# Kernel tuning notes

Hardware: AMD Instinct MI355X
Metric: run time of the kernel (lower is better)

Reference implementation:

```python
import jax, jax.numpy as jnp
import numpy as np
from jax import lax

EPS = 1e-5


def _conv3x3(x, w):
    # NCHW input, OIHW weight, stride 1, padding 1
    return lax.conv_general_dilated(
        x, w, window_strides=(1, 1), padding=((1, 1), (1, 1)),
        dimension_numbers=("NCHW", "OIHW", "NCHW"))


def _batchnorm(y, gamma, beta):
    # training-mode BN: batch statistics over N,H,W
    mean = jnp.mean(y, axis=(0, 2, 3), keepdims=True)
    var = jnp.var(y, axis=(0, 2, 3), keepdims=True)
    inv = lax.rsqrt(var + EPS)
    return (y - mean) * inv * gamma[None, :, None, None] + beta[None, :, None, None]


def setup_inputs() -> dict:
    key = jax.random.key(0)
    k1, k2, k3 = jax.random.split(key, 3)
    N, C, H, W = 32, 128, 56, 56
    x = jax.random.normal(k1, (N, C, H, W), dtype=jnp.float32)
    w1 = jax.random.normal(k2, (C, C, 3, 3), dtype=jnp.float32) * 0.05
    w2 = jax.random.normal(k3, (C, C, 3, 3), dtype=jnp.float32) * 0.05
    gamma1 = jnp.ones((C,), jnp.float32)
    beta1 = jnp.zeros((C,), jnp.float32)
    gamma2 = jnp.ones((C,), jnp.float32)
    beta2 = jnp.zeros((C,), jnp.float32)
    return {"x": x, "w1": w1, "gamma1": gamma1, "beta1": beta1,
            "w2": w2, "gamma2": gamma2, "beta2": beta2}


def reference(x, w1, gamma1, beta1, w2, gamma2, beta2):
    # binarized conv weights: sign(w), with straight-through estimator
    # (matches torch's .data swap, which routes grads to the original weight)
    w1b = w1 + lax.stop_gradient(jnp.sign(w1) - w1)
    w2b = w2 + lax.stop_gradient(jnp.sign(w2) - w2)
    out = jax.nn.relu(_batchnorm(_conv3x3(x, w1b), gamma1, beta1))
    out = _batchnorm(_conv3x3(out, w2b), gamma2, beta2)
    out = out + x  # identity shortcut (stride=1, in_planes==planes)
    return jax.nn.relu(out)
```

## Files before the change

### kernel.cpp

```cpp
#include <hip/hip_runtime.h>

typedef unsigned short u16;
typedef unsigned short u16x8 __attribute__((ext_vector_type(8)));
typedef __bf16 bf16x8 __attribute__((ext_vector_type(8)));
typedef float f32x4 __attribute__((ext_vector_type(4)));

#define HW 3136
#define NPIX 100352
#define PADR 3364
#define KD 1152

__device__ __forceinline__ float bf2f(u16 u) {
    unsigned int x = ((unsigned int)u) << 16;
    return __builtin_bit_cast(float, x);
}
__device__ __forceinline__ u16 f2bf(float f) {
    unsigned int u = __builtin_bit_cast(unsigned int, f);
    return (u16)((u + 0x7FFFu + ((u >> 16) & 1u)) >> 16);
}
__device__ __forceinline__ void gload16(const void* g, void* l) {
    __builtin_amdgcn_global_load_lds(
        (const __attribute__((address_space(1))) unsigned int*)g,
        (__attribute__((address_space(3))) unsigned int*)l, 16, 0, 0);
}

__global__ void setup_kernel(const float* __restrict__ w1, const float* __restrict__ w2,
                             u16* __restrict__ Bm1, u16* __restrict__ Bm2,
                             u16* __restrict__ xbp) {
    const int b = blockIdx.x;
    const int t = threadIdx.x;
    if (b < 1152) {
        const float* w = (b < 576) ? w1 : w2;
        u16* Bm = (b < 576) ? Bm1 : Bm2;
        int i = (b % 576) * 256 + t;
        int k  = i / KD;
        int kk = i - k * KD;
        int c  = kk & 127;
        int rs = kk >> 7;
        float v = w[(size_t)(k * 128 + c) * 9 + rs];
        float sv = (v > 0.f) ? 1.f : ((v < 0.f) ? -1.f : 0.f);
        Bm[i] = f2bf(sv);
    } else {
        int idx = (b - 1152) * 256 + t;
        int pix = idx >> 4;
        int cc  = idx & 15;
        int n  = pix / 228;
        int pb = pix - n * 228;
        int h, w;
        if (pb < 58)       { h = 0;  w = pb; }
        else if (pb < 116) { h = 57; w = pb - 58; }
        else { int q = pb - 116; h = 1 + (q >> 1); w = (q & 1) ? 57 : 0; }
        u16x8 z = {};
        *(u16x8*)(xbp + ((size_t)(n * PADR + h * 58 + w)) * 128 + cc * 8) = z;
    }
}

__global__ void x_to_nhwc(const float* __restrict__ x, u16* __restrict__ xbp) {
    __shared__ float tile[32][65];
    const int t = threadIdx.x;
    const int n = blockIdx.y;
    const int ct = blockIdx.x & 3;
    const int pt = blockIdx.x >> 2;
    const int c0 = ct * 32, p0 = pt * 64;
    {
        const int c  = t >> 3;
        const int pw = (t & 7) * 8;
        const size_t ib = ((size_t)(n * 128 + c0 + c)) * HW + p0 + pw;
        const float4 v0 = *(const float4*)(x + ib);
        const float4 v1 = *(const float4*)(x + ib + 4);
        tile[c][pw + 0] = v0.x; tile[c][pw + 1] = v0.y;
        tile[c][pw + 2] = v0.z; tile[c][pw + 3] = v0.w;
        tile[c][pw + 4] = v1.x; tile[c][pw + 5] = v1.y;
        tile[c][pw + 6] = v1.z; tile[c][pw + 7] = v1.w;
    }
    __syncthreads();
    {
        const int pl = t >> 2;
        const int cs = (t & 3) * 8;
        const int p  = p0 + pl;
        const int h  = p / 56;
        const int w  = p - h * 56;
        u16x8 o;
#pragma unroll
        for (int j = 0; j < 8; ++j) o[j] = f2bf(tile[cs + j][pl]);
        *(u16x8*)(xbp + ((size_t)(n * PADR + (h + 1) * 58 + (w + 1))) * 128 + c0 + cs) = o;
    }
}

#define A0 0
#define B0 8192
#define A1 16384
#define B1 24576

__global__ __launch_bounds__(256, 2) void conv_mfma(
    const u16* __restrict__ xbp, const u16* __restrict__ Bm,
    u16* __restrict__ y, float2* __restrict__ partial)
{
    __shared__ __align__(16) u16 smem[32768];
    const int t = threadIdx.x;
    const int bid = blockIdx.x;
    const int pm0 = bid * 128;
    const int wid  = t >> 6;
    const int lane = t & 63;
    const int lrow = lane & 15;
    const int lhk  = lane >> 4;
    const int m0 = (wid >> 1) * 64;
    const int n0 = (wid & 1) * 64;

    const int rsub = lane >> 3;
    const int csrc = (lane & 7) ^ rsub;
    int apix[4], bbase[4];
#pragma unroll
    for (int j = 0; j < 4; ++j) {
        int row = (wid * 4 + j) * 8 + rsub;
        int ps  = pm0 + row;
        int n   = ps / HW;
        int rem = ps - n * HW;
        int h   = rem / 56;
        int w   = rem - h * 56;
        apix[j]  = (n * PADR + (h + 1) * 58 + (w + 1)) * 128 + csrc * 8;
        bbase[j] = row * KD + csrc * 8;
    }

    f32x4 acc[4][4] = {};

#define STAGE(AOFF, BOFF, p) do {                                              \
    int rs_ = (p) >> 1; int r_ = rs_ / 3; int s_ = rs_ - r_ * 3;               \
    int ash = ((r_ - 1) * 58 + (s_ - 1)) * 128 + ((p) & 1) * 64;               \
    int bsh = (p) * 64;                                                        \
    _Pragma("unroll")                                                          \
    for (int j = 0; j < 4; ++j) {                                              \
        gload16(xbp + apix[j] + ash, smem + (AOFF) + (wid * 4 + j) * 512);     \
        gload16(Bm + bbase[j] + bsh, smem + (BOFF) + (wid * 4 + j) * 512);     \
    } } while (0)

#define COMPUTE(AOFF, BOFF) do {                                               \
    _Pragma("unroll")                                                          \
    for (int kc = 0; kc < 2; ++kc) {                                           \
        bf16x8 af[4], bv[4];                                                   \
        _Pragma("unroll")                                                      \
        for (int mi = 0; mi < 4; ++mi) {                                       \
            int ck = (((kc << 2) | lhk) ^ (lrow & 7)) << 3;                    \
            af[mi] = *(const bf16x8*)&smem[(AOFF) + (m0 + mi * 16 + lrow) * 64 + ck]; \
        }                                                                      \
        _Pragma("unroll")                                                      \
        for (int ni = 0; ni < 4; ++ni) {                                       \
            int ck = (((kc << 2) | lhk) ^ (lrow & 7)) << 3;                    \
            bv[ni] = *(const bf16x8*)&smem[(BOFF) + (n0 + ni * 16 + lrow) * 64 + ck]; \
        }                                                                      \
        __builtin_amdgcn_s_setprio(1);                                         \
        _Pragma("unroll")                                                      \
        for (int mi = 0; mi < 4; ++mi)                                         \
        _Pragma("unroll")                                                      \
            for (int ni = 0; ni < 4; ++ni)                                     \
                acc[mi][ni] = __builtin_amdgcn_mfma_f32_16x16x32_bf16(         \
                    af[mi], bv[ni], acc[mi][ni], 0, 0, 0);                     \
        __builtin_amdgcn_s_setprio(0);                                         \
    } } while (0)

    STAGE(A0, B0, 0);
    __syncthreads();
#pragma unroll 1
    for (int pp = 0; pp < 18; pp += 2) {
        STAGE(A1, B1, pp + 1);
        COMPUTE(A0, B0);
        __syncthreads();
        if (pp < 16) STAGE(A0, B0, pp + 2);
        COMPUTE(A1, B1);
        __syncthreads();
    }
#undef STAGE
#undef COMPUTE

    float sv[4], qv[4];
#pragma unroll
    for (int ni = 0; ni < 4; ++ni) {
        float a = 0.f, b = 0.f;
#pragma unroll
        for (int mi = 0; mi < 4; ++mi)
#pragma unroll
            for (int q = 0; q < 4; ++q) { float v = acc[mi][ni][q]; a += v; b += v * v; }
        a += __shfl_xor(a, 16); a += __shfl_xor(a, 32);
        b += __shfl_xor(b, 16); b += __shfl_xor(b, 32);
        sv[ni] = a; qv[ni] = b;
    }
    float2* sred = (float2*)(smem + 20480);
    if (lane < 16) {
#pragma unroll
        for (int ni = 0; ni < 4; ++ni)
            sred[wid * 64 + ni * 16 + lane] = make_float2(sv[ni], qv[ni]);
    }

#pragma unroll
    for (int mi = 0; mi < 4; ++mi)
#pragma unroll
        for (int ni = 0; ni < 4; ++ni)
#pragma unroll
            for (int q = 0; q < 4; ++q)
                smem[(m0 + mi * 16 + lhk * 4 + q) * 136 + n0 + ni * 16 + lrow] =
                    f2bf(acc[mi][ni][q]);
    __syncthreads();
    {
        const int px = t >> 1, half = t & 1;
        const u16* src = &smem[px * 136 + half * 64];
        u16* dst = y + (size_t)(pm0 + px) * 128 + half * 64;
#pragma unroll
        for (int j = 0; j < 8; ++j)
            *(u16x8*)(dst + j * 8) = *(const u16x8*)(src + j * 8);
    }
    if (t < 128) {
        const int ni = (t >> 4) & 3, oc = t & 15, hi = t >> 6;
        float2 u = sred[hi * 64 + ni * 16 + oc];
        float2 v = sred[(hi + 2) * 64 + ni * 16 + oc];
        partial[(size_t)t * 784 + bid] = make_float2(u.x + v.x, u.y + v.y);
    }
}

__global__ void stats_finalize(const float2* __restrict__ partial,
                               const float* __restrict__ gamma, const float* __restrict__ beta,
                               float2* __restrict__ coef) {
    __shared__ float ss[256], ss2[256];
    const int c = blockIdx.x, t = threadIdx.x;
    const float2* pc = partial + (size_t)c * 784;
    float s = 0.f, s2 = 0.f;
    for (int i = t; i < 784; i += 256) { float2 v = pc[i]; s += v.x; s2 += v.y; }
    ss[t] = s; ss2[t] = s2;
    __syncthreads();
    for (int o = 128; o > 0; o >>= 1) {
        if (t < o) { ss[t] += ss[t + o]; ss2[t] += ss2[t + o]; }
        __syncthreads();
    }
    if (t == 0) {
        double mean = (double)ss[0] / (double)NPIX;
        double var  = (double)ss2[0] / (double)NPIX - mean * mean;
        if (var < 0.0) var = 0.0;
        float inv = rsqrtf((float)var + 1e-5f);
        float a = gamma[c] * inv;
        coef[c] = make_float2(a, beta[c] - (float)mean * a);
    }
}

__global__ void bnrelu_kernel(const u16* __restrict__ y, const float2* __restrict__ coef,
                              u16* __restrict__ xbp) {
    __shared__ float2 sc[128];
    const int t = threadIdx.x;
    if (t < 128) sc[t] = coef[t];
    __syncthreads();
    size_t i = (size_t)blockIdx.x * 256 + t;
    u16x8 v = *(const u16x8*)(y + i * 8);
    int p  = (int)(i >> 4);
    int c0 = (int)(i & 15) * 8;
    int n   = p / HW;
    int rem = p - n * HW;
    int h   = rem / 56;
    int w   = rem - h * 56;
    u16x8 o;
#pragma unroll
    for (int j = 0; j < 8; ++j) {
        float2 k = sc[c0 + j];
        o[j] = f2bf(fmaxf(bf2f(v[j]) * k.x + k.y, 0.f));
    }
    *(u16x8*)(xbp + ((size_t)(n * PADR + (h + 1) * 58 + (w + 1))) * 128 + c0) = o;
}

__global__ void bn_add_relu_nchw(const u16* __restrict__ y2, const float2* __restrict__ coef,
                                 const float* __restrict__ x, float* __restrict__ out) {
    __shared__ float tile[32][65];
    __shared__ float2 sc[32];
    const int t = threadIdx.x;
    const int n = blockIdx.y;
    const int ct = blockIdx.x & 3;
    const int pt = blockIdx.x >> 2;
    const int c0 = ct * 32, p0 = pt * 64;
    if (t < 32) sc[t] = coef[c0 + t];
    __syncthreads();
    {
        const int p  = t >> 2;
        const int cs = (t & 3) * 8;
        const u16x8 v = *(const u16x8*)(y2 + ((size_t)(n * HW + p0 + p)) * 128 + c0 + cs);
#pragma unroll
        for (int j = 0; j < 8; ++j) {
            float2 k = sc[cs + j];
            tile[cs + j][p] = bf2f(v[j]) * k.x + k.y;
        }
    }
    __syncthreads();
    {
        const int c  = t >> 3;
        const int pw = (t & 7) * 8;
        const size_t ob = ((size_t)(n * 128 + c0 + c)) * HW + p0 + pw;
        const float4 x0 = *(const float4*)(x + ob);
        const float4 x1 = *(const float4*)(x + ob + 4);
        float4 o0, o1;
        o0.x = fmaxf(tile[c][pw + 0] + x0.x, 0.f);
        o0.y = fmaxf(tile[c][pw + 1] + x0.y, 0.f);
        o0.z = fmaxf(tile[c][pw + 2] + x0.z, 0.f);
        o0.w = fmaxf(tile[c][pw + 3] + x0.w, 0.f);
        o1.x = fmaxf(tile[c][pw + 4] + x1.x, 0.f);
        o1.y = fmaxf(tile[c][pw + 5] + x1.y, 0.f);
        o1.z = fmaxf(tile[c][pw + 6] + x1.z, 0.f);
        o1.w = fmaxf(tile[c][pw + 7] + x1.w, 0.f);
        *(float4*)(out + ob) = o0;
        *(float4*)(out + ob + 4) = o1;
    }
}

extern "C" void kernel_launch(void* const* d_in, const int* in_sizes, int n_in,
                              void* d_out, int out_size, void* d_ws, size_t ws_size,
                              hipStream_t stream) {
    const float* x  = (const float*)d_in[0];
    const float* w1 = (const float*)d_in[1];
    const float* g1 = (const float*)d_in[2];
    const float* b1 = (const float*)d_in[3];
    const float* w2 = (const float*)d_in[4];
    const float* g2 = (const float*)d_in[5];
    const float* b2 = (const float*)d_in[6];
    float* out = (float*)d_out;
    char* ws = (char*)d_ws;

    u16*    xbp  = (u16*)(ws);
    u16*    ybuf = (u16*)(ws + 27557888);
    u16*    Bm1  = (u16*)(ws + 53248000);
    u16*    Bm2  = (u16*)(ws + 53542912);
    float2* part = (float2*)(ws + 53837824);
    float2* cf1  = (float2*)(ws + 54640640);
    float2* cf2  = (float2*)(ws + 54641664);

    setup_kernel<<<1608, 256, 0, stream>>>(w1, w2, Bm1, Bm2, xbp);
    x_to_nhwc<<<dim3(196, 32), 256, 0, stream>>>(x, xbp);

    conv_mfma<<<784, 256, 0, stream>>>(xbp, Bm1, ybuf, part);
    stats_finalize<<<128, 256, 0, stream>>>(part, g1, b1, cf1);
    bnrelu_kernel<<<6272, 256, 0, stream>>>(ybuf, cf1, xbp);

    conv_mfma<<<784, 256, 0, stream>>>(xbp, Bm2, ybuf, part);
    stats_finalize<<<128, 256, 0, stream>>>(part, g2, b2, cf2);
    bn_add_relu_nchw<<<dim3(196, 32), 256, 0, stream>>>(ybuf, cf2, x, out);
}
```

Baseline: 148.5 us.

## Deepen conv LDS pipeline with vmcnt waits and read residual from bf16 NHWC

The conv main loop now keeps two stages of global_load_lds in flight. It uses explicit s_waitcnt vmcnt(8)/s_barrier pairs instead of __syncthreads, so loads for the next stage overlap the MFMA compute of the current one. The BN+ReLU intermediate is written into the output buffer as a padded scratch area, with extra blocks zeroing its border. This keeps the bf16 NHWC copy of x intact. The final kernel then reads the residual from that bf16 copy instead of the fp32 NCHW x, cutting memory traffic but adding bf16 rounding to the residual.

```diff
diff --git a/kernel.cpp b/kernel.cpp
--- a/kernel.cpp
+++ b/kernel.cpp
@@ -158,19 +158,34 @@
         __builtin_amdgcn_s_setprio(0);                                         \
     } } while (0)
 
+#define WAITBAR8() asm volatile("s_waitcnt vmcnt(8)\n\ts_barrier" ::: "memory")
+#define WAITBAR0() asm volatile("s_waitcnt vmcnt(0)\n\ts_barrier" ::: "memory")
+#define BAR()      asm volatile("s_barrier" ::: "memory")
+
     STAGE(A0, B0, 0);
-    __syncthreads();
+    STAGE(A1, B1, 1);
 #pragma unroll 1
-    for (int pp = 0; pp < 18; pp += 2) {
-        STAGE(A1, B1, pp + 1);
+    for (int pp = 0; pp < 16; pp += 2) {
+        WAITBAR8();
         COMPUTE(A0, B0);
-        __syncthreads();
-        if (pp < 16) STAGE(A0, B0, pp + 2);
+        BAR();
+        STAGE(A0, B0, pp + 2);
+        WAITBAR8();
         COMPUTE(A1, B1);
-        __syncthreads();
-    }
+        BAR();
+        STAGE(A1, B1, pp + 3);
+    }
+    WAITBAR8();
+    COMPUTE(A0, B0);
+    BAR();
+    WAITBAR0();
+    COMPUTE(A1, B1);
+    BAR();
 #undef STAGE
 #undef COMPUTE
+#undef WAITBAR8
+#undef WAITBAR0
+#undef BAR
 
     float sv[4], qv[4];
 #pragma unroll
@@ -241,12 +256,27 @@
 }
 
 __global__ void bnrelu_kernel(const u16* __restrict__ y, const float2* __restrict__ coef,
-                              u16* __restrict__ xbp) {
+                              u16* __restrict__ out1p) {
     __shared__ float2 sc[128];
-    const int t = threadIdx.x;
+    const int b = blockIdx.x;
+    const int t = threadIdx.x;
+    if (b >= 6272) {
+        int idx = (b - 6272) * 256 + t;
+        int pix = idx >> 4;
+        int cc  = idx & 15;
+        int n  = pix / 228;
+        int pb = pix - n * 228;
+        int h, w;
+        if (pb < 58)       { h = 0;  w = pb; }
+        else if (pb < 116) { h = 57; w = pb - 58; }
+        else { int q = pb - 116; h = 1 + (q >> 1); w = (q & 1) ? 57 : 0; }
+        u16x8 z = {};
+        *(u16x8*)(out1p + ((size_t)(n * PADR + h * 58 + w)) * 128 + cc * 8) = z;
+        return;
+    }
     if (t < 128) sc[t] = coef[t];
     __syncthreads();
-    size_t i = (size_t)blockIdx.x * 256 + t;
+    size_t i = (size_t)b * 256 + t;
     u16x8 v = *(const u16x8*)(y + i * 8);
     int p  = (int)(i >> 4);
     int c0 = (int)(i & 15) * 8;
@@ -260,11 +290,11 @@
         float2 k = sc[c0 + j];
         o[j] = f2bf(fmaxf(bf2f(v[j]) * k.x + k.y, 0.f));
     }
-    *(u16x8*)(xbp + ((size_t)(n * PADR + (h + 1) * 58 + (w + 1))) * 128 + c0) = o;
+    *(u16x8*)(out1p + ((size_t)(n * PADR + (h + 1) * 58 + (w + 1))) * 128 + c0) = o;
 }
 
 __global__ void bn_add_relu_nchw(const u16* __restrict__ y2, const float2* __restrict__ coef,
-                                 const float* __restrict__ x, float* __restrict__ out) {
+                                 const u16* __restrict__ xbp, float* __restrict__ out) {
     __shared__ float tile[32][65];
     __shared__ float2 sc[32];
     const int t = threadIdx.x;
@@ -275,13 +305,18 @@
     if (t < 32) sc[t] = coef[c0 + t];
     __syncthreads();
     {
-        const int p  = t >> 2;
+        const int pl = t >> 2;
         const int cs = (t & 3) * 8;
-        const u16x8 v = *(const u16x8*)(y2 + ((size_t)(n * HW + p0 + p)) * 128 + c0 + cs);
+        const int p  = p0 + pl;
+        const int h  = p / 56;
+        const int w  = p - h * 56;
+        const u16x8 v = *(const u16x8*)(y2 + ((size_t)(n * HW + p)) * 128 + c0 + cs);
+        const u16x8 xv = *(const u16x8*)(xbp +
+            ((size_t)(n * PADR + (h + 1) * 58 + (w + 1))) * 128 + c0 + cs);
 #pragma unroll
         for (int j = 0; j < 8; ++j) {
             float2 k = sc[cs + j];
-            tile[cs + j][p] = bf2f(v[j]) * k.x + k.y;
+            tile[cs + j][pl] = bf2f(v[j]) * k.x + k.y + bf2f(xv[j]);
         }
     }
     __syncthreads();
@@ -289,17 +324,15 @@
         const int c  = t >> 3;
         const int pw = (t & 7) * 8;
         const size_t ob = ((size_t)(n * 128 + c0 + c)) * HW + p0 + pw;
-        const float4 x0 = *(const float4*)(x + ob);
-        const float4 x1 = *(const float4*)(x + ob + 4);
         float4 o0, o1;
-        o0.x = fmaxf(tile[c][pw + 0] + x0.x, 0.f);
-        o0.y = fmaxf(tile[c][pw + 1] + x0.y, 0.f);
-        o0.z = fmaxf(tile[c][pw + 2] + x0.z, 0.f);
-        o0.w = fmaxf(tile[c][pw + 3] + x0.w, 0.f);
-        o1.x = fmaxf(tile[c][pw + 4] + x1.x, 0.f);
-        o1.y = fmaxf(tile[c][pw + 5] + x1.y, 0.f);
-        o1.z = fmaxf(tile[c][pw + 6] + x1.z, 0.f);
-        o1.w = fmaxf(tile[c][pw + 7] + x1.w, 0.f);
+        o0.x = fmaxf(tile[c][pw + 0], 0.f);
+        o0.y = fmaxf(tile[c][pw + 1], 0.f);
+        o0.z = fmaxf(tile[c][pw + 2], 0.f);
+        o0.w = fmaxf(tile[c][pw + 3], 0.f);
+        o1.x = fmaxf(tile[c][pw + 4], 0.f);
+        o1.y = fmaxf(tile[c][pw + 5], 0.f);
+        o1.z = fmaxf(tile[c][pw + 6], 0.f);
+        o1.w = fmaxf(tile[c][pw + 7], 0.f);
         *(float4*)(out + ob) = o0;
         *(float4*)(out + ob + 4) = o1;
     }
@@ -318,22 +351,23 @@
     float* out = (float*)d_out;
     char* ws = (char*)d_ws;
 
-    u16*    xbp  = (u16*)(ws);
-    u16*    ybuf = (u16*)(ws + 27557888);
-    u16*    Bm1  = (u16*)(ws + 53248000);
-    u16*    Bm2  = (u16*)(ws + 53542912);
-    float2* part = (float2*)(ws + 53837824);
-    float2* cf1  = (float2*)(ws + 54640640);
-    float2* cf2  = (float2*)(ws + 54641664);
+    u16*    xbp   = (u16*)(ws);
+    u16*    ybuf  = (u16*)(ws + 27557888);
+    u16*    Bm1   = (u16*)(ws + 53248000);
+    u16*    Bm2   = (u16*)(ws + 53542912);
+    float2* part  = (float2*)(ws + 53837824);
+    float2* cf1   = (float2*)(ws + 54640640);
+    float2* cf2   = (float2*)(ws + 54641664);
+    u16*    out1p = (u16*)d_out;
 
     setup_kernel<<<1608, 256, 0, stream>>>(w1, w2, Bm1, Bm2, xbp);
     x_to_nhwc<<<dim3(196, 32), 256, 0, stream>>>(x, xbp);
 
     conv_mfma<<<784, 256, 0, stream>>>(xbp, Bm1, ybuf, part);
     stats_finalize<<<128, 256, 0, stream>>>(part, g1, b1, cf1);
-    bnrelu_kernel<<<6272, 256, 0, stream>>>(ybuf, cf1, xbp);
-
-    conv_mfma<<<784, 256, 0, stream>>>(xbp, Bm2, ybuf, part);
+    bnrelu_kernel<<<6728, 256, 0, stream>>>(ybuf, cf1, out1p);
+
+    conv_mfma<<<784, 256, 0, stream>>>(out1p, Bm2, ybuf, part);
     stats_finalize<<<128, 256, 0, stream>>>(part, g2, b2, cf2);
-    bn_add_relu_nchw<<<dim3(196, 32), 256, 0, stream>>>(ybuf, cf2, x, out);
-}
+    bn_add_relu_nchw<<<dim3(196, 32), 256, 0, stream>>>(ybuf, cf2, xbp, out);
+}
```

Measured after the change: 150.1 us. Within noise of the previous version (+1.1%).
